# Optimization experiments

Hardware: AMD Instinct MI355X
Metric: run time of the kernel (lower is better)

The kernel has to match this reference:

```python
import jax, jax.numpy as jnp
import numpy as np

N_TASKS = 3
N_SHARED = 4
N_TASK = 2
INP = 1024
EXPERT_DIM = 512


def setup_inputs() -> dict:
    key = jax.random.key(0)
    ks = jax.random.split(key, 7)
    s = 0.02
    task_inputs = jax.random.normal(ks[0], (N_TASKS, 16384, INP), dtype=jnp.float32)
    shared_W = jax.random.normal(ks[1], (N_SHARED, INP, EXPERT_DIM), dtype=jnp.float32) * s
    shared_b = jnp.zeros((N_SHARED, EXPERT_DIM), dtype=jnp.float32)
    task_W = jax.random.normal(ks[2], (N_TASKS, N_TASK, INP, EXPERT_DIM), dtype=jnp.float32) * s
    task_b = jnp.zeros((N_TASKS, N_TASK, EXPERT_DIM), dtype=jnp.float32)
    gate_W = jax.random.normal(ks[3], (N_TASKS, INP, N_SHARED + N_TASK), dtype=jnp.float32) * s
    gate_b = jnp.zeros((N_TASKS, N_SHARED + N_TASK), dtype=jnp.float32)
    return {
        'task_inputs': task_inputs,
        'shared_W': shared_W, 'shared_b': shared_b,
        'task_W': task_W, 'task_b': task_b,
        'gate_W': gate_W, 'gate_b': gate_b,
    }


def reference(task_inputs, shared_W, shared_b, task_W, task_b, gate_W, gate_b):
    # task_inputs: [T, B, I]
    x0 = task_inputs[0]  # shared experts always see task 0's input
    # shared experts: [B, E_s, O]
    shared_outs = jax.nn.relu(jnp.einsum('bi,eio->beo', x0, shared_W) + shared_b)
    # per-task experts: [T, B, E_t, O]
    task_outs = jax.nn.relu(jnp.einsum('tbi,teio->tbeo', task_inputs, task_W) + task_b[:, None, :, :])
    # stack shared + task experts -> [T, B, E_s+E_t, O]
    T = task_inputs.shape[0]
    all_outs = jnp.concatenate([
        jnp.broadcast_to(shared_outs[None], (T,) + shared_outs.shape),
        task_outs,
    ], axis=2)
    # gates: softmax over experts, [T, B, E_s+E_t]
    g = jax.nn.softmax(jnp.einsum('tbi,tig->tbg', task_inputs, gate_W) + gate_b[:, None, :], axis=-1)
    # gated weighted sum over experts -> [T, B, O]
    return jnp.einsum('tbeo,tbe->tbo', all_outs, g)
```

## Files before the change

kernel.cpp:

```cpp
#include <hip/hip_runtime.h>
#include <hip/hip_bf16.h>
#include <stdint.h>


#define TTASKS 3
#define BROWS  16384
#define KDIM   1024
#define ODIM   512
#define NGATE  6

typedef __attribute__((ext_vector_type(8))) __bf16 bf16x8;
typedef __attribute__((ext_vector_type(4))) float  f32x4;

#define XB_OFF 0
#define WT_OFF 100663296UL
#define GT_OFF 111149056UL
#define SH_OFF 112328704UL

__global__ __launch_bounds__(256) void cvt_inputs(const float* __restrict__ x,
                                                  __bf16* __restrict__ xb) {
  size_t i = ((size_t)blockIdx.x * 256 + threadIdx.x) * 8;
  const float4* p = (const float4*)(x + i);
  float4 a = p[0], b = p[1];
  bf16x8 o = { (__bf16)a.x, (__bf16)a.y, (__bf16)a.z, (__bf16)a.w,
               (__bf16)b.x, (__bf16)b.y, (__bf16)b.z, (__bf16)b.w };
  *(bf16x8*)(xb + i) = o;
}

__global__ __launch_bounds__(256) void cvt_weights(const float* __restrict__ shW,
                                                   const float* __restrict__ tkW,
                                                   __bf16* __restrict__ wT) {
  int s = blockIdx.z;
  const float* src = (s < 4) ? (shW + (size_t)s * KDIM * ODIM)
                             : (tkW + (size_t)(s - 4) * KDIM * ODIM);
  int o   = blockIdx.x * 64 + (threadIdx.x & 63);
  int sub = threadIdx.x >> 6;
#pragma unroll
  for (int kk = 0; kk < 2; ++kk) {
    int k0 = blockIdx.y * 64 + (sub * 2 + kk) * 8;
    bf16x8 v;
#pragma unroll
    for (int i = 0; i < 8; ++i)
      v[i] = (__bf16)src[(size_t)(k0 + i) * ODIM + o];
    *(bf16x8*)(wT + ((size_t)s * ODIM + o) * KDIM + k0) = v;
  }
}

__global__ __launch_bounds__(256) void gates_kernel(const float* __restrict__ x,
                                                    const float* __restrict__ gW,
                                                    const float* __restrict__ gb,
                                                    float* __restrict__ gates) {
  int w = blockIdx.x * 4 + (threadIdx.x >> 6);
  int lane = threadIdx.x & 63;
  int t = w >> 14, b = w & (BROWS - 1);
  const float* xr = x + ((size_t)t * BROWS + b) * KDIM;
  const float* gw = gW + (size_t)t * KDIM * NGATE;
  float d[NGATE] = {0.f, 0.f, 0.f, 0.f, 0.f, 0.f};
  for (int i = 0; i < 16; ++i) {
    int k = i * 64 + lane;
    float xv = xr[k];
#pragma unroll
    for (int j = 0; j < NGATE; ++j) d[j] += xv * gw[k * NGATE + j];
  }
#pragma unroll
  for (int j = 0; j < NGATE; ++j) {
#pragma unroll
    for (int off = 32; off > 0; off >>= 1) d[j] += __shfl_xor(d[j], off, 64);
    d[j] += gb[t * NGATE + j];
  }
  float m = d[0];
#pragma unroll
  for (int j = 1; j < NGATE; ++j) m = fmaxf(m, d[j]);
  float s = 0.f;
#pragma unroll
  for (int j = 0; j < NGATE; ++j) { d[j] = expf(d[j] - m); s += d[j]; }
  float inv = 1.f / s;
  if (lane < NGATE) {
    float v = d[0];
#pragma unroll
    for (int j = 1; j < NGATE; ++j) v = (lane == j) ? d[j] : v;
    gates[(size_t)w * NGATE + lane] = v * inv;
  }
}

__device__ __forceinline__ void gemm_128x128(const __bf16* __restrict__ Aptr,
                                             const __bf16* __restrict__ Bptr,
                                             __bf16* As, __bf16* Bs,
                                             f32x4 acc[4][4]) {
  const int tid = threadIdx.x;
  const int lane = tid & 63;
  const int wv = tid >> 6;
  const int wm = wv >> 1, wn = wv & 1;
  const int lr = lane & 15, lg = lane >> 4;

  for (int kt = 0; kt < 16; ++kt) {
    const int k0 = kt * 64;
#pragma unroll
    for (int it = 0; it < 4; ++it) {
      int idx = it * 256 + tid;
      int r   = idx >> 3;
      int c8  = (idx & 7) << 3;
      __builtin_amdgcn_global_load_lds(
          (const __attribute__((address_space(1))) void*)(Aptr + (size_t)r * KDIM + k0 + c8),
          (__attribute__((address_space(3))) void*)(As + (it * 256 + wv * 64) * 8), 16, 0, 0);
      __builtin_amdgcn_global_load_lds(
          (const __attribute__((address_space(1))) void*)(Bptr + (size_t)r * KDIM + k0 + c8),
          (__attribute__((address_space(3))) void*)(Bs + (it * 256 + wv * 64) * 8), 16, 0, 0);
    }
    __syncthreads();

    const __bf16* aB = As + (wm * 64 + lr) * 64 + lg * 8;
    const __bf16* bB = Bs + (wn * 64 + lr) * 64 + lg * 8;
#pragma unroll
    for (int ks = 0; ks < 2; ++ks) {
      bf16x8 af[4], bf[4];
#pragma unroll
      for (int m = 0; m < 4; ++m) af[m] = *(const bf16x8*)(aB + m * 1024 + ks * 32);
#pragma unroll
      for (int n = 0; n < 4; ++n) bf[n] = *(const bf16x8*)(bB + n * 1024 + ks * 32);
#pragma unroll
      for (int m = 0; m < 4; ++m)
#pragma unroll
        for (int n = 0; n < 4; ++n)
          acc[m][n] = __builtin_amdgcn_mfma_f32_16x16x32_bf16(af[m], bf[n], acc[m][n], 0, 0, 0);
    }
    __syncthreads();
  }
}

__global__ __launch_bounds__(256, 2) void shared_gemm(const __bf16* __restrict__ xb0,
                                                      const __bf16* __restrict__ wT,
                                                      const float* __restrict__ shb,
                                                      __bf16* __restrict__ shOut) {
  __shared__ __bf16 As[128 * 64], Bs[128 * 64];
  const int e = blockIdx.z;
  const int rowBase = blockIdx.x * 128, colBase = blockIdx.y * 128;
  const int tid = threadIdx.x, lane = tid & 63, wv = tid >> 6;
  const int wm = wv >> 1, wn = wv & 1, lr = lane & 15, lg = lane >> 4;

  f32x4 acc[4][4];
  f32x4 z = {0.f, 0.f, 0.f, 0.f};
#pragma unroll
  for (int m = 0; m < 4; ++m)
#pragma unroll
    for (int n = 0; n < 4; ++n) acc[m][n] = z;

  gemm_128x128(xb0 + (size_t)rowBase * KDIM,
               wT + ((size_t)e * ODIM + colBase) * KDIM, As, Bs, acc);

#pragma unroll
  for (int n = 0; n < 4; ++n) {
    int col = colBase + wn * 64 + n * 16 + lr;
    float bias = shb[e * ODIM + col];
#pragma unroll
    for (int m = 0; m < 4; ++m)
#pragma unroll
      for (int r = 0; r < 4; ++r) {
        int row = rowBase + wm * 64 + m * 16 + lg * 4 + r;
        float v = fmaxf(acc[m][n][r] + bias, 0.f);
        shOut[((size_t)e * BROWS + row) * ODIM + col] = (__bf16)v;
      }
  }
}

__global__ __launch_bounds__(256, 2) void task_gemm(const __bf16* __restrict__ xb,
                                                    const __bf16* __restrict__ wT,
                                                    const float* __restrict__ tkb,
                                                    const float* __restrict__ gates,
                                                    const __bf16* __restrict__ shOut,
                                                    float* __restrict__ out) {
  __shared__ __bf16 As[128 * 64], Bs[128 * 64];
  const int t = blockIdx.z;
  const int rowBase = blockIdx.x * 128, colBase = blockIdx.y * 128;
  const int tid = threadIdx.x, lane = tid & 63, wv = tid >> 6;
  const int wm = wv >> 1, wn = wv & 1, lr = lane & 15, lg = lane >> 4;

  float outv[4][4][4];

#pragma unroll
  for (int m = 0; m < 4; ++m)
#pragma unroll
    for (int r = 0; r < 4; ++r) {
      int row = rowBase + wm * 64 + m * 16 + lg * 4 + r;
      const float* gp = gates + ((size_t)t * BROWS + row) * NGATE;
      float g0 = gp[0], g1 = gp[1], g2 = gp[2], g3 = gp[3];
#pragma unroll
      for (int n = 0; n < 4; ++n) {
        int col = colBase + wn * 64 + n * 16 + lr;
        size_t rc = (size_t)row * ODIM + col;
        float s = g0 * (float)shOut[rc]
                + g1 * (float)shOut[(size_t)BROWS * ODIM + rc]
                + g2 * (float)shOut[2 * (size_t)BROWS * ODIM + rc]
                + g3 * (float)shOut[3 * (size_t)BROWS * ODIM + rc];
        outv[m][n][r] = s;
      }
    }

#pragma unroll 1
  for (int j = 0; j < 2; ++j) {
    f32x4 acc[4][4];
    f32x4 z = {0.f, 0.f, 0.f, 0.f};
#pragma unroll
    for (int m = 0; m < 4; ++m)
#pragma unroll
      for (int n = 0; n < 4; ++n) acc[m][n] = z;

    gemm_128x128(xb + ((size_t)t * BROWS + rowBase) * KDIM,
                 wT + ((size_t)(4 + t * 2 + j) * ODIM + colBase) * KDIM, As, Bs, acc);

#pragma unroll
    for (int n = 0; n < 4; ++n) {
      int col = colBase + wn * 64 + n * 16 + lr;
      float bias = tkb[(t * 2 + j) * ODIM + col];
#pragma unroll
      for (int m = 0; m < 4; ++m)
#pragma unroll
        for (int r = 0; r < 4; ++r) {
          int row = rowBase + wm * 64 + m * 16 + lg * 4 + r;
          float g = gates[((size_t)t * BROWS + row) * NGATE + 4 + j];
          outv[m][n][r] += g * fmaxf(acc[m][n][r] + bias, 0.f);
        }
    }
  }

#pragma unroll
  for (int n = 0; n < 4; ++n) {
    int col = colBase + wn * 64 + n * 16 + lr;
#pragma unroll
    for (int m = 0; m < 4; ++m)
#pragma unroll
      for (int r = 0; r < 4; ++r) {
        int row = rowBase + wm * 64 + m * 16 + lg * 4 + r;
        out[((size_t)t * BROWS + row) * ODIM + col] = outv[m][n][r];
      }
  }
}

extern "C" void kernel_launch(void* const* d_in, const int* in_sizes, int n_in,
                              void* d_out, int out_size, void* d_ws, size_t ws_size,
                              hipStream_t stream) {
  const float* x   = (const float*)d_in[0];
  const float* shW = (const float*)d_in[1];
  const float* shb = (const float*)d_in[2];
  const float* tkW = (const float*)d_in[3];
  const float* tkb = (const float*)d_in[4];
  const float* gW  = (const float*)d_in[5];
  const float* gb  = (const float*)d_in[6];
  float* out = (float*)d_out;
  (void)in_sizes; (void)n_in; (void)out_size; (void)ws_size;

  char* ws = (char*)d_ws;
  __bf16* xb    = (__bf16*)(ws + XB_OFF);
  __bf16* wT    = (__bf16*)(ws + WT_OFF);
  float*  gates = (float*) (ws + GT_OFF);
  __bf16* shOut = (__bf16*)(ws + SH_OFF);

  cvt_inputs <<<dim3(24576), 256, 0, stream>>>(x, xb);
  cvt_weights<<<dim3(8, 16, 10), 256, 0, stream>>>(shW, tkW, wT);
  gates_kernel<<<dim3((TTASKS * BROWS) / 4), 256, 0, stream>>>(x, gW, gb, gates);

  shared_gemm<<<dim3(BROWS / 128, ODIM / 128, 4), 256, 0, stream>>>(xb, wT, shb, shOut);

  task_gemm<<<dim3(BROWS / 128, ODIM / 128, TTASKS), 256, 0, stream>>>(xb, wT, tkb, gates,
                                                                       shOut, out);
}
```

Measured before the change: 677.1 us.

## Rewrite GEMMs as 8-wave 256x128 tiles with double-buffered swizzled LDS

Replaces the 128x128 single-buffered GEMM with a 512-thread, 256x128-tile core. It double-buffers A and B in LDS with an XOR swizzle to avoid bank conflicts, splits each K step into two MFMA phases, and uses explicit waitcnt, barriers and setprio to overlap loads with compute. The task GEMM becomes two kernels, one per task expert. The second kernel does a read-modify-write on the fp32 output, which adds output traffic but lowers register pressure and increases parallelism.

```diff
diff --git a/kernel.cpp b/kernel.cpp
--- a/kernel.cpp
+++ b/kernel.cpp
@@ -8,6 +8,8 @@
 #define KDIM   1024
 #define ODIM   512
 #define NGATE  6
+#define BK     64
+#define NT     (KDIM / BK)
 
 typedef __attribute__((ext_vector_type(8))) __bf16 bf16x8;
 typedef __attribute__((ext_vector_type(4))) float  f32x4;
@@ -16,6 +18,14 @@
 #define WT_OFF 100663296UL
 #define GT_OFF 111149056UL
 #define SH_OFF 112328704UL
+
+#define MFMA_(a, bb, c) __builtin_amdgcn_mfma_f32_16x16x32_bf16(a, bb, c, 0, 0, 0)
+
+__device__ __forceinline__ void BAR() {
+  asm volatile("" ::: "memory");
+  __builtin_amdgcn_s_barrier();
+  asm volatile("" ::: "memory");
+}
 
 __global__ __launch_bounds__(256) void cvt_inputs(const float* __restrict__ x,
                                                   __bf16* __restrict__ xb) {
@@ -83,157 +93,217 @@
   }
 }
 
-__device__ __forceinline__ void gemm_128x128(const __bf16* __restrict__ Aptr,
-                                             const __bf16* __restrict__ Bptr,
-                                             __bf16* As, __bf16* Bs,
-                                             f32x4 acc[4][4]) {
-  const int tid = threadIdx.x;
-  const int lane = tid & 63;
+__device__ __forceinline__ void stage_half(const __bf16* __restrict__ g,
+                                           __bf16* lds, int h, int tid) {
   const int wv = tid >> 6;
+#pragma unroll
+  for (int l = 0; l < 2; ++l) {
+    const int idx = l * 512 + tid;
+    const int r   = h * 128 + (idx >> 3);
+    const int cs  = (idx & 7) ^ (r & 7);
+    __builtin_amdgcn_global_load_lds(
+        (const __attribute__((address_space(1))) void*)(g + (size_t)r * KDIM + cs * 8),
+        (__attribute__((address_space(3))) void*)(lds + h * 8192 + (l * 512 + wv * 64) * 8),
+        16, 0, 0);
+  }
+}
+
+__device__ __forceinline__ void gemm_core(const __bf16* __restrict__ Ap,
+                                          const __bf16* __restrict__ Bp,
+                                          __bf16 (*As_)[256 * 64],
+                                          __bf16 (*Bs_)[128 * 64],
+                                          f32x4 acc[4][4]) {
+  const int tid = threadIdx.x, lane = tid & 63, wv = tid >> 6;
   const int wm = wv >> 1, wn = wv & 1;
-  const int lr = lane & 15, lg = lane >> 4;
-
-  for (int kt = 0; kt < 16; ++kt) {
-    const int k0 = kt * 64;
-#pragma unroll
-    for (int it = 0; it < 4; ++it) {
-      int idx = it * 256 + tid;
-      int r   = idx >> 3;
-      int c8  = (idx & 7) << 3;
-      __builtin_amdgcn_global_load_lds(
-          (const __attribute__((address_space(1))) void*)(Aptr + (size_t)r * KDIM + k0 + c8),
-          (__attribute__((address_space(3))) void*)(As + (it * 256 + wv * 64) * 8), 16, 0, 0);
-      __builtin_amdgcn_global_load_lds(
-          (const __attribute__((address_space(1))) void*)(Bptr + (size_t)r * KDIM + k0 + c8),
-          (__attribute__((address_space(3))) void*)(Bs + (it * 256 + wv * 64) * 8), 16, 0, 0);
-    }
-    __syncthreads();
-
-    const __bf16* aB = As + (wm * 64 + lr) * 64 + lg * 8;
-    const __bf16* bB = Bs + (wn * 64 + lr) * 64 + lg * 8;
-#pragma unroll
-    for (int ks = 0; ks < 2; ++ks) {
-      bf16x8 af[4], bf[4];
-#pragma unroll
-      for (int m = 0; m < 4; ++m) af[m] = *(const bf16x8*)(aB + m * 1024 + ks * 32);
-#pragma unroll
-      for (int n = 0; n < 4; ++n) bf[n] = *(const bf16x8*)(bB + n * 1024 + ks * 32);
-#pragma unroll
-      for (int m = 0; m < 4; ++m)
-#pragma unroll
-        for (int n = 0; n < 4; ++n)
-          acc[m][n] = __builtin_amdgcn_mfma_f32_16x16x32_bf16(af[m], bf[n], acc[m][n], 0, 0, 0);
-    }
-    __syncthreads();
-  }
-}
-
-__global__ __launch_bounds__(256, 2) void shared_gemm(const __bf16* __restrict__ xb0,
-                                                      const __bf16* __restrict__ wT,
-                                                      const float* __restrict__ shb,
-                                                      __bf16* __restrict__ shOut) {
-  __shared__ __bf16 As[128 * 64], Bs[128 * 64];
+  const int lr = lane & 15, lg = lane >> 4, x7 = lr & 7;
+
+  stage_half(Ap,          As_[0], 0, tid);
+  stage_half(Ap,          As_[0], 1, tid);
+  stage_half(Bp,          Bs_[0], 0, tid);
+  stage_half(Bp + BK,     Bs_[1], 0, tid);
+  asm volatile("s_waitcnt vmcnt(2)" ::: "memory");
+  BAR();
+
+  for (int t = 0; t < NT; ++t) {
+    const int b = t & 1;
+    const __bf16* Ab = As_[b];
+    const __bf16* Bb = Bs_[b];
+
+    bf16x8 bF[4][2];
+#pragma unroll
+    for (int ni = 0; ni < 4; ++ni)
+#pragma unroll
+      for (int ks = 0; ks < 2; ++ks)
+        bF[ni][ks] = *(const bf16x8*)(Bb + (wn * 64 + ni * 16 + lr) * 64 +
+                                      (((ks * 4 + lg) ^ x7) * 8));
+    bf16x8 a0[2][2];
+#pragma unroll
+    for (int mi = 0; mi < 2; ++mi)
+#pragma unroll
+      for (int ks = 0; ks < 2; ++ks)
+        a0[mi][ks] = *(const bf16x8*)(Ab + (wm * 64 + mi * 16 + lr) * 64 +
+                                      (((ks * 4 + lg) ^ x7) * 8));
+    if (t + 1 < NT) {
+      stage_half(Ap + (t + 1) * BK, As_[(t + 1) & 1], 0, tid);
+      stage_half(Ap + (t + 1) * BK, As_[(t + 1) & 1], 1, tid);
+    }
+    BAR();
+    asm volatile("s_waitcnt lgkmcnt(0)" ::: "memory");
+    __builtin_amdgcn_s_setprio(1);
+#pragma unroll
+    for (int ni = 0; ni < 4; ++ni) {
+      acc[0][ni] = MFMA_(a0[0][0], bF[ni][0], acc[0][ni]);
+      acc[0][ni] = MFMA_(a0[0][1], bF[ni][1], acc[0][ni]);
+      acc[1][ni] = MFMA_(a0[1][0], bF[ni][0], acc[1][ni]);
+      acc[1][ni] = MFMA_(a0[1][1], bF[ni][1], acc[1][ni]);
+    }
+    __builtin_amdgcn_s_setprio(0);
+    BAR();
+
+    bf16x8 a1[2][2];
+#pragma unroll
+    for (int mi = 0; mi < 2; ++mi)
+#pragma unroll
+      for (int ks = 0; ks < 2; ++ks)
+        a1[mi][ks] = *(const bf16x8*)(Ab + (wm * 64 + (mi + 2) * 16 + lr) * 64 +
+                                      (((ks * 4 + lg) ^ x7) * 8));
+    if (t + 2 < NT) {
+      stage_half(Bp + (t + 2) * BK, Bs_[b], 0, tid);
+      asm volatile("s_waitcnt vmcnt(2)" ::: "memory");
+    } else {
+      asm volatile("s_waitcnt vmcnt(0)" ::: "memory");
+    }
+    BAR();
+    asm volatile("s_waitcnt lgkmcnt(0)" ::: "memory");
+    __builtin_amdgcn_s_setprio(1);
+#pragma unroll
+    for (int ni = 0; ni < 4; ++ni) {
+      acc[2][ni] = MFMA_(a1[0][0], bF[ni][0], acc[2][ni]);
+      acc[2][ni] = MFMA_(a1[0][1], bF[ni][1], acc[2][ni]);
+      acc[3][ni] = MFMA_(a1[1][0], bF[ni][0], acc[3][ni]);
+      acc[3][ni] = MFMA_(a1[1][1], bF[ni][1], acc[3][ni]);
+    }
+    __builtin_amdgcn_s_setprio(0);
+    BAR();
+  }
+}
+
+__global__ __launch_bounds__(512, 2) void shared_gemm8(const __bf16* __restrict__ xb0,
+                                                       const __bf16* __restrict__ wT,
+                                                       const float* __restrict__ shb,
+                                                       __bf16* __restrict__ shOut) {
+  __shared__ __align__(16) __bf16 As_[2][256 * 64];
+  __shared__ __align__(16) __bf16 Bs_[2][128 * 64];
   const int e = blockIdx.z;
-  const int rowBase = blockIdx.x * 128, colBase = blockIdx.y * 128;
+  const int rowBase = blockIdx.x * 256, colBase = blockIdx.y * 128;
   const int tid = threadIdx.x, lane = tid & 63, wv = tid >> 6;
   const int wm = wv >> 1, wn = wv & 1, lr = lane & 15, lg = lane >> 4;
 
   f32x4 acc[4][4];
   f32x4 z = {0.f, 0.f, 0.f, 0.f};
 #pragma unroll
-  for (int m = 0; m < 4; ++m)
-#pragma unroll
-    for (int n = 0; n < 4; ++n) acc[m][n] = z;
-
-  gemm_128x128(xb0 + (size_t)rowBase * KDIM,
-               wT + ((size_t)e * ODIM + colBase) * KDIM, As, Bs, acc);
-
-#pragma unroll
-  for (int n = 0; n < 4; ++n) {
-    int col = colBase + wn * 64 + n * 16 + lr;
+  for (int mi = 0; mi < 4; ++mi)
+#pragma unroll
+    for (int ni = 0; ni < 4; ++ni) acc[mi][ni] = z;
+
+  gemm_core(xb0 + (size_t)rowBase * KDIM,
+            wT + ((size_t)e * ODIM + colBase) * KDIM, As_, Bs_, acc);
+
+#pragma unroll
+  for (int ni = 0; ni < 4; ++ni) {
+    int col = colBase + wn * 64 + ni * 16 + lr;
     float bias = shb[e * ODIM + col];
 #pragma unroll
-    for (int m = 0; m < 4; ++m)
+    for (int mi = 0; mi < 4; ++mi)
 #pragma unroll
       for (int r = 0; r < 4; ++r) {
-        int row = rowBase + wm * 64 + m * 16 + lg * 4 + r;
-        float v = fmaxf(acc[m][n][r] + bias, 0.f);
+        int row = rowBase + wm * 64 + mi * 16 + lg * 4 + r;
+        float v = fmaxf(acc[mi][ni][r] + bias, 0.f);
         shOut[((size_t)e * BROWS + row) * ODIM + col] = (__bf16)v;
       }
   }
 }
 
-__global__ __launch_bounds__(256, 2) void task_gemm(const __bf16* __restrict__ xb,
-                                                    const __bf16* __restrict__ wT,
-                                                    const float* __restrict__ tkb,
-                                                    const float* __restrict__ gates,
-                                                    const __bf16* __restrict__ shOut,
-                                                    float* __restrict__ out) {
-  __shared__ __bf16 As[128 * 64], Bs[128 * 64];
+__global__ __launch_bounds__(512, 2) void taskA_gemm8(const __bf16* __restrict__ xb,
+                                                      const __bf16* __restrict__ wT,
+                                                      const float* __restrict__ tkb,
+                                                      const float* __restrict__ gates,
+                                                      const __bf16* __restrict__ shOut,
+                                                      float* __restrict__ out) {
+  __shared__ __align__(16) __bf16 As_[2][256 * 64];
+  __shared__ __align__(16) __bf16 Bs_[2][128 * 64];
   const int t = blockIdx.z;
-  const int rowBase = blockIdx.x * 128, colBase = blockIdx.y * 128;
+  const int rowBase = blockIdx.x * 256, colBase = blockIdx.y * 128;
   const int tid = threadIdx.x, lane = tid & 63, wv = tid >> 6;
   const int wm = wv >> 1, wn = wv & 1, lr = lane & 15, lg = lane >> 4;
-
-  float outv[4][4][4];
-
-#pragma unroll
-  for (int m = 0; m < 4; ++m)
+  const size_t NB = (size_t)BROWS * ODIM;
+
+  f32x4 acc[4][4];
+  f32x4 z = {0.f, 0.f, 0.f, 0.f};
+#pragma unroll
+  for (int mi = 0; mi < 4; ++mi)
+#pragma unroll
+    for (int ni = 0; ni < 4; ++ni) acc[mi][ni] = z;
+
+  gemm_core(xb + ((size_t)t * BROWS + rowBase) * KDIM,
+            wT + ((size_t)(4 + t * 2) * ODIM + colBase) * KDIM, As_, Bs_, acc);
+
+#pragma unroll
+  for (int mi = 0; mi < 4; ++mi)
 #pragma unroll
     for (int r = 0; r < 4; ++r) {
-      int row = rowBase + wm * 64 + m * 16 + lg * 4 + r;
+      int row = rowBase + wm * 64 + mi * 16 + lg * 4 + r;
       const float* gp = gates + ((size_t)t * BROWS + row) * NGATE;
-      float g0 = gp[0], g1 = gp[1], g2 = gp[2], g3 = gp[3];
-#pragma unroll
-      for (int n = 0; n < 4; ++n) {
-        int col = colBase + wn * 64 + n * 16 + lr;
+      float g0 = gp[0], g1 = gp[1], g2 = gp[2], g3 = gp[3], g4 = gp[4];
+#pragma unroll
+      for (int ni = 0; ni < 4; ++ni) {
+        int col = colBase + wn * 64 + ni * 16 + lr;
         size_t rc = (size_t)row * ODIM + col;
-        float s = g0 * (float)shOut[rc]
-                + g1 * (float)shOut[(size_t)BROWS * ODIM + rc]
-                + g2 * (float)shOut[2 * (size_t)BROWS * ODIM + rc]
-                + g3 * (float)shOut[3 * (size_t)BROWS * ODIM + rc];
-        outv[m][n][r] = s;
+        float s = g0 * (float)shOut[rc] + g1 * (float)shOut[NB + rc] +
+                  g2 * (float)shOut[2 * NB + rc] + g3 * (float)shOut[3 * NB + rc];
+        float bias = tkb[(t * 2) * ODIM + col];
+        s += g4 * fmaxf(acc[mi][ni][r] + bias, 0.f);
+        out[((size_t)t * BROWS + row) * ODIM + col] = s;
       }
     }
-
-#pragma unroll 1
-  for (int j = 0; j < 2; ++j) {
-    f32x4 acc[4][4];
-    f32x4 z = {0.f, 0.f, 0.f, 0.f};
-#pragma unroll
-    for (int m = 0; m < 4; ++m)
-#pragma unroll
-      for (int n = 0; n < 4; ++n) acc[m][n] = z;
-
-    gemm_128x128(xb + ((size_t)t * BROWS + rowBase) * KDIM,
-                 wT + ((size_t)(4 + t * 2 + j) * ODIM + colBase) * KDIM, As, Bs, acc);
-
-#pragma unroll
-    for (int n = 0; n < 4; ++n) {
-      int col = colBase + wn * 64 + n * 16 + lr;
-      float bias = tkb[(t * 2 + j) * ODIM + col];
-#pragma unroll
-      for (int m = 0; m < 4; ++m)
-#pragma unroll
-        for (int r = 0; r < 4; ++r) {
-          int row = rowBase + wm * 64 + m * 16 + lg * 4 + r;
-          float g = gates[((size_t)t * BROWS + row) * NGATE + 4 + j];
-          outv[m][n][r] += g * fmaxf(acc[m][n][r] + bias, 0.f);
-        }
-    }
-  }
-
-#pragma unroll
-  for (int n = 0; n < 4; ++n) {
-    int col = colBase + wn * 64 + n * 16 + lr;
-#pragma unroll
-    for (int m = 0; m < 4; ++m)
-#pragma unroll
-      for (int r = 0; r < 4; ++r) {
-        int row = rowBase + wm * 64 + m * 16 + lg * 4 + r;
-        out[((size_t)t * BROWS + row) * ODIM + col] = outv[m][n][r];
+}
+
+__global__ __launch_bounds__(512, 2) void taskB_gemm8(const __bf16* __restrict__ xb,
+                                                      const __bf16* __restrict__ wT,
+                                                      const float* __restrict__ tkb,
+                                                      const float* __restrict__ gates,
+                                                      float* __restrict__ out) {
+  __shared__ __align__(16) __bf16 As_[2][256 * 64];
+  __shared__ __align__(16) __bf16 Bs_[2][128 * 64];
+  const int t = blockIdx.z;
+  const int rowBase = blockIdx.x * 256, colBase = blockIdx.y * 128;
+  const int tid = threadIdx.x, lane = tid & 63, wv = tid >> 6;
+  const int wm = wv >> 1, wn = wv & 1, lr = lane & 15, lg = lane >> 4;
+
+  f32x4 acc[4][4];
+  f32x4 z = {0.f, 0.f, 0.f, 0.f};
+#pragma unroll
+  for (int mi = 0; mi < 4; ++mi)
+#pragma unroll
+    for (int ni = 0; ni < 4; ++ni) acc[mi][ni] = z;
+
+  gemm_core(xb + ((size_t)t * BROWS + rowBase) * KDIM,
+            wT + ((size_t)(4 + t * 2 + 1) * ODIM + colBase) * KDIM, As_, Bs_, acc);
+
+#pragma unroll
+  for (int mi = 0; mi < 4; ++mi)
+#pragma unroll
+    for (int r = 0; r < 4; ++r) {
+      int row = rowBase + wm * 64 + mi * 16 + lg * 4 + r;
+      float g5 = gates[((size_t)t * BROWS + row) * NGATE + 5];
+#pragma unroll
+      for (int ni = 0; ni < 4; ++ni) {
+        int col = colBase + wn * 64 + ni * 16 + lr;
+        float bias = tkb[(t * 2 + 1) * ODIM + col];
+        size_t oi = ((size_t)t * BROWS + row) * ODIM + col;
+        out[oi] += g5 * fmaxf(acc[mi][ni][r] + bias, 0.f);
       }
-  }
+    }
 }
 
 extern "C" void kernel_launch(void* const* d_in, const int* in_sizes, int n_in,
@@ -259,8 +329,9 @@
   cvt_weights<<<dim3(8, 16, 10), 256, 0, stream>>>(shW, tkW, wT);
   gates_kernel<<<dim3((TTASKS * BROWS) / 4), 256, 0, stream>>>(x, gW, gb, gates);
 
-  shared_gemm<<<dim3(BROWS / 128, ODIM / 128, 4), 256, 0, stream>>>(xb, wT, shb, shOut);
-
-  task_gemm<<<dim3(BROWS / 128, ODIM / 128, TTASKS), 256, 0, stream>>>(xb, wT, tkb, gates,
-                                                                       shOut, out);
-}
+  shared_gemm8<<<dim3(BROWS / 256, ODIM / 128, 4), 512, 0, stream>>>(xb, wT, shb, shOut);
+  taskA_gemm8 <<<dim3(BROWS / 256, ODIM / 128, TTASKS), 512, 0, stream>>>(xb, wT, tkb, gates,
+                                                                          shOut, out);
+  taskB_gemm8 <<<dim3(BROWS / 256, ODIM / 128, TTASKS), 512, 0, stream>>>(xb, wT, tkb, gates,
+                                                                          out);
+}
```

Result: slower. 727.6 us (+7.5%).
